# Optimization experiments

Hardware: AMD Instinct MI355X
Metric: run time of the kernel (lower is better)

The kernel has to match this reference:

```python
import jax, jax.numpy as jnp
import numpy as np

N_QUBITS = 4
N_LAYERS = 2
DIM = 2 ** N_QUBITS  # 16
B = 65536


def _apply_1q(state, U, wire):
    # state: (B,) + (2,)*N_QUBITS complex64; U: (2,2) complex. Wire 0 = most significant (PennyLane order).
    s = jnp.moveaxis(state, wire + 1, -1)
    s = jnp.einsum('...j,ij->...i', s, U)
    return jnp.moveaxis(s, -1, wire + 1)


def _apply_cnot(state, control, target):
    s = jnp.moveaxis(state, (control + 1, target + 1), (-2, -1))
    s = jnp.concatenate([s[..., 0:1, :], s[..., 1:2, ::-1]], axis=-2)
    return jnp.moveaxis(s, (-2, -1), (control + 1, target + 1))


def _rot_matrix(phi, th, om):
    # qml.Rot(phi, theta, omega) = RZ(om) RY(th) RZ(phi)
    c = jnp.cos(th / 2)
    sn = jnp.sin(th / 2)
    ep = jnp.exp(-0.5j * (phi + om).astype(jnp.complex64))
    em = jnp.exp(0.5j * (phi - om).astype(jnp.complex64))
    row0 = jnp.stack([ep * c, -em * sn])
    row1 = jnp.stack([jnp.conj(em) * sn, jnp.conj(ep) * c])
    return jnp.stack([row0, row1])


def _strongly_entangling(state, theta):
    # PennyLane StronglyEntanglingLayers, default ranges r_l = (l % (n-1)) + 1, CNOT imprimitive ring
    for l in range(N_LAYERS):
        for w in range(N_QUBITS):
            U = _rot_matrix(theta[l, w, 0], theta[l, w, 1], theta[l, w, 2])
            state = _apply_1q(state, U, w)
        r = (l % (N_QUBITS - 1)) + 1
        for w in range(N_QUBITS):
            state = _apply_cnot(state, w, (w + r) % N_QUBITS)
    return state


def _encode(x, W1, b1, W2, b2):
    v = x.reshape(x.shape[0], -1) @ W1 + b1
    v = jax.nn.relu(v)
    v = v @ W2 + b2
    v = jnp.nan_to_num(v, nan=0.0, posinf=1.0, neginf=-1.0)
    v = jnp.tanh(v)
    nrm = jnp.linalg.norm(v, axis=-1, keepdims=True)
    return v / jnp.maximum(nrm, 1e-8)  # F.normalize(p=2, eps=1e-8)


def _prepare_state(v, theta):
    # AmplitudeEmbedding(normalize=True): renormalize, embed as amplitudes
    v = v / jnp.linalg.norm(v, axis=-1, keepdims=True)
    state = v.astype(jnp.complex64).reshape((v.shape[0],) + (2,) * N_QUBITS)
    return _strongly_entangling(state, theta)


def setup_inputs() -> dict:
    key = jax.random.key(0)
    k = jax.random.split(key, 7)
    return {
        'img_a': jax.random.normal(k[0], (B, 1, 28, 28), dtype=jnp.float32),
        'img_b': jax.random.normal(k[1], (B, 1, 28, 28), dtype=jnp.float32),
        'W1': 0.05 * jax.random.normal(k[2], (784, 64), dtype=jnp.float32),
        'b1': 0.05 * jax.random.normal(k[3], (64,), dtype=jnp.float32),
        'W2': 0.05 * jax.random.normal(k[4], (64, 16), dtype=jnp.float32),
        'b2': 0.05 * jax.random.normal(k[5], (16,), dtype=jnp.float32),
        'theta': 0.05 * jax.random.normal(k[6], (N_LAYERS, N_QUBITS, 3), dtype=jnp.float32),
    }


def reference(img_a, img_b, W1, b1, W2, b2, theta):
    theta_safe = jnp.nan_to_num(theta, nan=0.0, posinf=1.0, neginf=-1.0)
    va = _encode(img_a, W1, b1, W2, b2)
    vb = _encode(img_b, W1, b1, W2, b2)
    sa = _prepare_state(va, theta_safe).reshape(-1, DIM)
    sb = _prepare_state(vb, theta_safe).reshape(-1, DIM)
    # SWAP test: p0 = (1 + |<a|b>|^2)/2  =>  clamp(2*p0 - 1, 0, 1) = clip(|<a|b>|^2, 0, 1)
    ov = jnp.einsum('bd,bd->b', jnp.conj(sa), sb)
    fid = jnp.clip(jnp.abs(ov) ** 2, 0.0, 1.0)
    return fid.astype(jnp.float32)
```

## Files before the change

### kernel.cpp

```cpp
#include <hip/hip_runtime.h>


#define KDIM   784
#define HDIM   64
#define KSTEPS 25
#define W1S_ELEMS (KSTEPS * 4 * 64 * 8)
#define W1S_BYTES (W1S_ELEMS * 2)

typedef float  f32x4  __attribute__((ext_vector_type(4)));
typedef short  bf16x8 __attribute__((ext_vector_type(8)));

__device__ __forceinline__ unsigned short f2bf(float f) {
  unsigned u = __float_as_uint(f);
  u += 0x7fffu + ((u >> 16) & 1u);
  return (unsigned short)(u >> 16);
}

__device__ __forceinline__ float bf2f(unsigned short h) {
  return __uint_as_float(((unsigned)h) << 16);
}

__device__ __forceinline__ bf16x8 cvt8(f32x4 lo, f32x4 hi) {
  bf16x8 r;
  r[0] = (short)f2bf(lo[0]); r[1] = (short)f2bf(lo[1]);
  r[2] = (short)f2bf(lo[2]); r[3] = (short)f2bf(lo[3]);
  r[4] = (short)f2bf(hi[0]); r[5] = (short)f2bf(hi[1]);
  r[6] = (short)f2bf(hi[2]); r[7] = (short)f2bf(hi[3]);
  return r;
}

__device__ __forceinline__ float tanh_fast(float x) {
  float e = __expf(2.0f * x);
  return 1.0f - 2.0f / (e + 1.0f);
}

__global__ __launch_bounds__(256)
void prep_kernel(const float* __restrict__ W1, const float* __restrict__ W2,
                 unsigned short* __restrict__ w1s, float* __restrict__ w2t) {
  int tid = blockIdx.x * 256 + threadIdx.x;
  if (tid < W1S_ELEMS) {
    int j  = tid & 7;
    int l  = (tid >> 3) & 63;
    int st = tid >> 9;
    int s  = st >> 2;
    int t  = st & 3;
    int k  = s * 32 + (l >> 4) * 8 + j;
    int n  = t * 16 + (l & 15);
    float v = (k < KDIM) ? W1[k * HDIM + n] : 0.0f;
    w1s[tid] = f2bf(v);
  }
  if (tid < HDIM * 16) {
    int c = tid >> 6;
    int k = tid & 63;
    w2t[c * HDIM + k] = W2[k * 16 + c];
  }
}

__global__ __launch_bounds__(256, 4)
void qcm_kernel(const float* __restrict__ img_a, const float* __restrict__ img_b,
                const float* __restrict__ b1,    const float* __restrict__ b2,
                const unsigned short* __restrict__ w1s,
                const float* __restrict__ w2t,
                float* __restrict__ out) {
  __shared__ __attribute__((aligned(16))) unsigned short lds_h[128][72];

  const int tid  = threadIdx.x;
  const int wave = tid >> 6;
  const int lane = tid & 63;
  const int m    = lane & 15;
  const int quad = lane >> 4;
  const int p0   = blockIdx.x * 64 + wave * 16;

  const float* rowA = img_a + (size_t)(p0 + m) * KDIM;
  const float* rowB = img_b + (size_t)(p0 + m) * KDIM;
  const int koff = quad * 8;

  f32x4 accA[4], accB[4];
  #pragma unroll
  for (int t = 0; t < 4; ++t) {
    accA[t][0] = accA[t][1] = accA[t][2] = accA[t][3] = 0.0f;
    accB[t][0] = accB[t][1] = accB[t][2] = accB[t][3] = 0.0f;
  }

  const int4* bwl = (const int4*)w1s + lane;
  f32x4 z4; z4[0] = z4[1] = z4[2] = z4[3] = 0.0f;

  f32x4 c0 = *(const f32x4*)(rowA + koff);
  f32x4 c1 = *(const f32x4*)(rowA + koff + 4);
  f32x4 c2 = *(const f32x4*)(rowB + koff);
  f32x4 c3 = *(const f32x4*)(rowB + koff + 4);

  for (int s = 0; s < KSTEPS; ++s) {
    int4 w0 = bwl[s * 256];
    int4 w1 = bwl[s * 256 + 64];
    int4 w2 = bwl[s * 256 + 128];
    int4 w3 = bwl[s * 256 + 192];

    f32x4 n0 = z4, n1 = z4, n2 = z4, n3 = z4;
    if (s < 23) {
      const int kb = (s + 1) * 32 + koff;
      n0 = *(const f32x4*)(rowA + kb);
      n1 = *(const f32x4*)(rowA + kb + 4);
      n2 = *(const f32x4*)(rowB + kb);
      n3 = *(const f32x4*)(rowB + kb + 4);
    } else if (s == 23) {
      if (quad < 2) {
        const int kb = 768 + koff;
        n0 = *(const f32x4*)(rowA + kb);
        n1 = *(const f32x4*)(rowA + kb + 4);
        n2 = *(const f32x4*)(rowB + kb);
        n3 = *(const f32x4*)(rowB + kb + 4);
      }
    }

    bf16x8 fa = cvt8(c0, c1);
    bf16x8 fb = cvt8(c2, c3);

    bf16x8 wf0 = __builtin_bit_cast(bf16x8, w0);
    bf16x8 wf1 = __builtin_bit_cast(bf16x8, w1);
    bf16x8 wf2 = __builtin_bit_cast(bf16x8, w2);
    bf16x8 wf3 = __builtin_bit_cast(bf16x8, w3);
    accA[0] = __builtin_amdgcn_mfma_f32_16x16x32_bf16(fa, wf0, accA[0], 0, 0, 0);
    accB[0] = __builtin_amdgcn_mfma_f32_16x16x32_bf16(fb, wf0, accB[0], 0, 0, 0);
    accA[1] = __builtin_amdgcn_mfma_f32_16x16x32_bf16(fa, wf1, accA[1], 0, 0, 0);
    accB[1] = __builtin_amdgcn_mfma_f32_16x16x32_bf16(fb, wf1, accB[1], 0, 0, 0);
    accA[2] = __builtin_amdgcn_mfma_f32_16x16x32_bf16(fa, wf2, accA[2], 0, 0, 0);
    accB[2] = __builtin_amdgcn_mfma_f32_16x16x32_bf16(fb, wf2, accB[2], 0, 0, 0);
    accA[3] = __builtin_amdgcn_mfma_f32_16x16x32_bf16(fa, wf3, accA[3], 0, 0, 0);
    accB[3] = __builtin_amdgcn_mfma_f32_16x16x32_bf16(fb, wf3, accB[3], 0, 0, 0);

    c0 = n0; c1 = n1; c2 = n2; c3 = n3;
  }

  #pragma unroll
  for (int t = 0; t < 4; ++t) {
    float bias = b1[t * 16 + m];
    const int ra = wave * 32;
    #pragma unroll
    for (int j = 0; j < 4; ++j) {
      float ha = fmaxf(accA[t][j] + bias, 0.0f);
      float hb = fmaxf(accB[t][j] + bias, 0.0f);
      lds_h[ra +      quad * 4 + j][t * 16 + m] = f2bf(ha);
      lds_h[ra + 16 + quad * 4 + j][t * 16 + m] = f2bf(hb);
    }
  }
  __syncthreads();

  const int p = tid >> 2;
  const int q = tid & 3;
  const int wsrc = p >> 4;
  const int r = p & 15;
  const unsigned short* ha_row = &lds_h[wsrc * 32 + r][0];
  const unsigned short* hb_row = &lds_h[wsrc * 32 + 16 + r][0];

  float za[4], zb[4];
  #pragma unroll
  for (int i = 0; i < 4; ++i) { za[i] = b2[q * 4 + i]; zb[i] = za[i]; }

  for (int k = 0; k < HDIM; k += 4) {
    uint2 ua = *(const uint2*)(ha_row + k);
    uint2 ub = *(const uint2*)(hb_row + k);
    float a0 = bf2f((unsigned short)(ua.x & 0xffff));
    float a1 = bf2f((unsigned short)(ua.x >> 16));
    float a2 = bf2f((unsigned short)(ua.y & 0xffff));
    float a3 = bf2f((unsigned short)(ua.y >> 16));
    float b0v = bf2f((unsigned short)(ub.x & 0xffff));
    float b1v = bf2f((unsigned short)(ub.x >> 16));
    float b2v = bf2f((unsigned short)(ub.y & 0xffff));
    float b3v = bf2f((unsigned short)(ub.y >> 16));
    #pragma unroll
    for (int i = 0; i < 4; ++i) {
      f32x4 wv = *(const f32x4*)(w2t + (q * 4 + i) * HDIM + k);
      za[i] += a0 * wv[0] + a1 * wv[1] + a2 * wv[2] + a3 * wv[3];
      zb[i] += b0v * wv[0] + b1v * wv[1] + b2v * wv[2] + b3v * wv[3];
    }
  }

  float d = 0.0f, na2 = 0.0f, nb2 = 0.0f;
  #pragma unroll
  for (int i = 0; i < 4; ++i) {
    float ua = tanh_fast(za[i]);
    float ub = tanh_fast(zb[i]);
    d   += ua * ub;
    na2 += ua * ua;
    nb2 += ub * ub;
  }
  d   += __shfl_xor(d, 1);   d   += __shfl_xor(d, 2);
  na2 += __shfl_xor(na2, 1); na2 += __shfl_xor(na2, 2);
  nb2 += __shfl_xor(nb2, 1); nb2 += __shfl_xor(nb2, 2);

  if (q == 0) {
    float den = fmaxf(sqrtf(na2), 1e-8f) * fmaxf(sqrtf(nb2), 1e-8f);
    float ov  = d / den;
    float fid = ov * ov;
    out[blockIdx.x * 64 + p] = fminf(fid, 1.0f);
  }
}

extern "C" void kernel_launch(void* const* d_in, const int* in_sizes, int n_in,
                              void* d_out, int out_size, void* d_ws, size_t ws_size,
                              hipStream_t stream) {
  const float* img_a = (const float*)d_in[0];
  const float* img_b = (const float*)d_in[1];
  const float* W1    = (const float*)d_in[2];
  const float* b1    = (const float*)d_in[3];
  const float* W2    = (const float*)d_in[4];
  const float* b2    = (const float*)d_in[5];

  unsigned short* w1s = (unsigned short*)d_ws;
  float* w2t = (float*)((char*)d_ws + W1S_BYTES);

  prep_kernel<<<(W1S_ELEMS + 255) / 256, 256, 0, stream>>>(W1, W2, w1s, w2t);

  const int n_pairs = out_size;
  qcm_kernel<<<n_pairs / 64, 256, 0, stream>>>(img_a, img_b, b1, b2, w1s, w2t,
                                               (float*)d_out);
}
```

Measured before the change: 116.9 us.

## Pack A and B rows into one MFMA tile to halve per-wave work

Each wave now handles 8 pairs, putting the img_a rows in MFMA rows 0-7 and the img_b rows in rows 8-15. That halves the accumulators and in-flight loads per thread, and launch bounds are raised to 8 blocks per CU with twice as many blocks. The aim is more occupancy and memory parallelism for this bandwidth-bound stream of images. The trade-off is twice the W1 fragment loads from cache per pair, and the second-layer stage is re-split over 8 threads per pair.

```diff
diff --git a/kernel.cpp b/kernel.cpp
--- a/kernel.cpp
+++ b/kernel.cpp
@@ -56,39 +56,36 @@
   }
 }
 
-__global__ __launch_bounds__(256, 4)
+__global__ __launch_bounds__(256, 8)
 void qcm_kernel(const float* __restrict__ img_a, const float* __restrict__ img_b,
                 const float* __restrict__ b1,    const float* __restrict__ b2,
                 const unsigned short* __restrict__ w1s,
                 const float* __restrict__ w2t,
                 float* __restrict__ out) {
-  __shared__ __attribute__((aligned(16))) unsigned short lds_h[128][72];
+  __shared__ __attribute__((aligned(16))) unsigned short lds_h[64][72];
 
   const int tid  = threadIdx.x;
   const int wave = tid >> 6;
   const int lane = tid & 63;
   const int m    = lane & 15;
   const int quad = lane >> 4;
-  const int p0   = blockIdx.x * 64 + wave * 16;
-
-  const float* rowA = img_a + (size_t)(p0 + m) * KDIM;
-  const float* rowB = img_b + (size_t)(p0 + m) * KDIM;
+  const int p0   = blockIdx.x * 32 + wave * 8;
+
+  const float* row = (m < 8)
+      ? (img_a + (size_t)(p0 + m)     * KDIM)
+      : (img_b + (size_t)(p0 + m - 8) * KDIM);
   const int koff = quad * 8;
 
-  f32x4 accA[4], accB[4];
+  f32x4 acc[4];
   #pragma unroll
-  for (int t = 0; t < 4; ++t) {
-    accA[t][0] = accA[t][1] = accA[t][2] = accA[t][3] = 0.0f;
-    accB[t][0] = accB[t][1] = accB[t][2] = accB[t][3] = 0.0f;
-  }
+  for (int t = 0; t < 4; ++t)
+    acc[t][0] = acc[t][1] = acc[t][2] = acc[t][3] = 0.0f;
 
   const int4* bwl = (const int4*)w1s + lane;
   f32x4 z4; z4[0] = z4[1] = z4[2] = z4[3] = 0.0f;
 
-  f32x4 c0 = *(const f32x4*)(rowA + koff);
-  f32x4 c1 = *(const f32x4*)(rowA + koff + 4);
-  f32x4 c2 = *(const f32x4*)(rowB + koff);
-  f32x4 c3 = *(const f32x4*)(rowB + koff + 4);
+  f32x4 c0 = *(const f32x4*)(row + koff);
+  f32x4 c1 = *(const f32x4*)(row + koff + 4);
 
   for (int s = 0; s < KSTEPS; ++s) {
     int4 w0 = bwl[s * 256];
@@ -96,66 +93,53 @@
     int4 w2 = bwl[s * 256 + 128];
     int4 w3 = bwl[s * 256 + 192];
 
-    f32x4 n0 = z4, n1 = z4, n2 = z4, n3 = z4;
+    f32x4 n0 = z4, n1 = z4;
     if (s < 23) {
       const int kb = (s + 1) * 32 + koff;
-      n0 = *(const f32x4*)(rowA + kb);
-      n1 = *(const f32x4*)(rowA + kb + 4);
-      n2 = *(const f32x4*)(rowB + kb);
-      n3 = *(const f32x4*)(rowB + kb + 4);
+      n0 = *(const f32x4*)(row + kb);
+      n1 = *(const f32x4*)(row + kb + 4);
     } else if (s == 23) {
       if (quad < 2) {
-        const int kb = 768 + koff;
-        n0 = *(const f32x4*)(rowA + kb);
-        n1 = *(const f32x4*)(rowA + kb + 4);
-        n2 = *(const f32x4*)(rowB + kb);
-        n3 = *(const f32x4*)(rowB + kb + 4);
+        n0 = *(const f32x4*)(row + 768 + koff);
+        n1 = *(const f32x4*)(row + 768 + koff + 4);
       }
     }
 
     bf16x8 fa = cvt8(c0, c1);
-    bf16x8 fb = cvt8(c2, c3);
-
-    bf16x8 wf0 = __builtin_bit_cast(bf16x8, w0);
-    bf16x8 wf1 = __builtin_bit_cast(bf16x8, w1);
-    bf16x8 wf2 = __builtin_bit_cast(bf16x8, w2);
-    bf16x8 wf3 = __builtin_bit_cast(bf16x8, w3);
-    accA[0] = __builtin_amdgcn_mfma_f32_16x16x32_bf16(fa, wf0, accA[0], 0, 0, 0);
-    accB[0] = __builtin_amdgcn_mfma_f32_16x16x32_bf16(fb, wf0, accB[0], 0, 0, 0);
-    accA[1] = __builtin_amdgcn_mfma_f32_16x16x32_bf16(fa, wf1, accA[1], 0, 0, 0);
-    accB[1] = __builtin_amdgcn_mfma_f32_16x16x32_bf16(fb, wf1, accB[1], 0, 0, 0);
-    accA[2] = __builtin_amdgcn_mfma_f32_16x16x32_bf16(fa, wf2, accA[2], 0, 0, 0);
-    accB[2] = __builtin_amdgcn_mfma_f32_16x16x32_bf16(fb, wf2, accB[2], 0, 0, 0);
-    accA[3] = __builtin_amdgcn_mfma_f32_16x16x32_bf16(fa, wf3, accA[3], 0, 0, 0);
-    accB[3] = __builtin_amdgcn_mfma_f32_16x16x32_bf16(fb, wf3, accB[3], 0, 0, 0);
-
-    c0 = n0; c1 = n1; c2 = n2; c3 = n3;
+
+    acc[0] = __builtin_amdgcn_mfma_f32_16x16x32_bf16(
+        fa, __builtin_bit_cast(bf16x8, w0), acc[0], 0, 0, 0);
+    acc[1] = __builtin_amdgcn_mfma_f32_16x16x32_bf16(
+        fa, __builtin_bit_cast(bf16x8, w1), acc[1], 0, 0, 0);
+    acc[2] = __builtin_amdgcn_mfma_f32_16x16x32_bf16(
+        fa, __builtin_bit_cast(bf16x8, w2), acc[2], 0, 0, 0);
+    acc[3] = __builtin_amdgcn_mfma_f32_16x16x32_bf16(
+        fa, __builtin_bit_cast(bf16x8, w3), acc[3], 0, 0, 0);
+
+    c0 = n0; c1 = n1;
   }
 
   #pragma unroll
   for (int t = 0; t < 4; ++t) {
     float bias = b1[t * 16 + m];
-    const int ra = wave * 32;
     #pragma unroll
     for (int j = 0; j < 4; ++j) {
-      float ha = fmaxf(accA[t][j] + bias, 0.0f);
-      float hb = fmaxf(accB[t][j] + bias, 0.0f);
-      lds_h[ra +      quad * 4 + j][t * 16 + m] = f2bf(ha);
-      lds_h[ra + 16 + quad * 4 + j][t * 16 + m] = f2bf(hb);
+      float h = fmaxf(acc[t][j] + bias, 0.0f);
+      lds_h[wave * 16 + quad * 4 + j][t * 16 + m] = f2bf(h);
     }
   }
   __syncthreads();
 
-  const int p = tid >> 2;
-  const int q = tid & 3;
-  const int wsrc = p >> 4;
-  const int r = p & 15;
-  const unsigned short* ha_row = &lds_h[wsrc * 32 + r][0];
-  const unsigned short* hb_row = &lds_h[wsrc * 32 + 16 + r][0];
-
-  float za[4], zb[4];
-  #pragma unroll
-  for (int i = 0; i < 4; ++i) { za[i] = b2[q * 4 + i]; zb[i] = za[i]; }
+  const int p = tid >> 3;
+  const int q = tid & 7;
+  const int wsrc = p >> 3;
+  const int r = p & 7;
+  const unsigned short* ha_row = &lds_h[wsrc * 16 + r][0];
+  const unsigned short* hb_row = &lds_h[wsrc * 16 + 8 + r][0];
+
+  float za[2], zb[2];
+  za[0] = b2[q * 2];     zb[0] = za[0];
+  za[1] = b2[q * 2 + 1]; zb[1] = za[1];
 
   for (int k = 0; k < HDIM; k += 4) {
     uint2 ua = *(const uint2*)(ha_row + k);
@@ -169,8 +153,8 @@
     float b2v = bf2f((unsigned short)(ub.y & 0xffff));
     float b3v = bf2f((unsigned short)(ub.y >> 16));
     #pragma unroll
-    for (int i = 0; i < 4; ++i) {
-      f32x4 wv = *(const f32x4*)(w2t + (q * 4 + i) * HDIM + k);
+    for (int i = 0; i < 2; ++i) {
+      f32x4 wv = *(const f32x4*)(w2t + (q * 2 + i) * HDIM + k);
       za[i] += a0 * wv[0] + a1 * wv[1] + a2 * wv[2] + a3 * wv[3];
       zb[i] += b0v * wv[0] + b1v * wv[1] + b2v * wv[2] + b3v * wv[3];
     }
@@ -178,22 +162,22 @@
 
   float d = 0.0f, na2 = 0.0f, nb2 = 0.0f;
   #pragma unroll
-  for (int i = 0; i < 4; ++i) {
+  for (int i = 0; i < 2; ++i) {
     float ua = tanh_fast(za[i]);
     float ub = tanh_fast(zb[i]);
     d   += ua * ub;
     na2 += ua * ua;
     nb2 += ub * ub;
   }
-  d   += __shfl_xor(d, 1);   d   += __shfl_xor(d, 2);
-  na2 += __shfl_xor(na2, 1); na2 += __shfl_xor(na2, 2);
-  nb2 += __shfl_xor(nb2, 1); nb2 += __shfl_xor(nb2, 2);
+  d   += __shfl_xor(d, 1);   d   += __shfl_xor(d, 2);   d   += __shfl_xor(d, 4);
+  na2 += __shfl_xor(na2, 1); na2 += __shfl_xor(na2, 2); na2 += __shfl_xor(na2, 4);
+  nb2 += __shfl_xor(nb2, 1); nb2 += __shfl_xor(nb2, 2); nb2 += __shfl_xor(nb2, 4);
 
   if (q == 0) {
     float den = fmaxf(sqrtf(na2), 1e-8f) * fmaxf(sqrtf(nb2), 1e-8f);
     float ov  = d / den;
     float fid = ov * ov;
-    out[blockIdx.x * 64 + p] = fminf(fid, 1.0f);
+    out[blockIdx.x * 32 + p] = fminf(fid, 1.0f);
   }
 }
 
@@ -213,6 +197,6 @@
   prep_kernel<<<(W1S_ELEMS + 255) / 256, 256, 0, stream>>>(W1, W2, w1s, w2t);
 
   const int n_pairs = out_size;
-  qcm_kernel<<<n_pairs / 64, 256, 0, stream>>>(img_a, img_b, b1, b2, w1s, w2t,
+  qcm_kernel<<<n_pairs / 32, 256, 0, stream>>>(img_a, img_b, b1, b2, w1s, w2t,
                                                (float*)d_out);
 }
```

New measurement: 134.7 us. 15.3% more time.

## Stage bf16 W1 tiles in LDS per 1024-thread block and deepen input prefetch

Applied to the files above, without the earlier changes.

Blocks grow from 256 to 1024 threads. Each block first copies the whole pre-swizzled bf16 W1 (about 100KB) into shared memory, and the MFMA loop reads weight fragments from LDS instead of global or L2 memory. The image-row loads are now prefetched two k-steps ahead. The goal is to cut repeated global weight traffic and hide input load latency in a memory-bound GEMV-like pass. In exchange, the large LDS footprint limits each CU to one block, and every block pays a prologue copy plus a barrier before streaming begins.

```diff
diff --git a/kernel.cpp b/kernel.cpp
--- a/kernel.cpp
+++ b/kernel.cpp
@@ -6,6 +6,7 @@
 #define KSTEPS 25
 #define W1S_ELEMS (KSTEPS * 4 * 64 * 8)
 #define W1S_BYTES (W1S_ELEMS * 2)
+#define W1S_INT4  (W1S_BYTES / 16)
 
 typedef float  f32x4  __attribute__((ext_vector_type(4)));
 typedef short  bf16x8 __attribute__((ext_vector_type(8)));
@@ -32,6 +33,30 @@
 __device__ __forceinline__ float tanh_fast(float x) {
   float e = __expf(2.0f * x);
   return 1.0f - 2.0f / (e + 1.0f);
+}
+
+__device__ __forceinline__ void load_a(const float* __restrict__ rowA,
+                                       const float* __restrict__ rowB,
+                                       int st, int koff, int quad,
+                                       f32x4& r0, f32x4& r1,
+                                       f32x4& r2, f32x4& r3) {
+  f32x4 z; z[0] = z[1] = z[2] = z[3] = 0.0f;
+  r0 = r1 = r2 = r3 = z;
+  if (st < 24) {
+    const int kb = st * 32 + koff;
+    r0 = *(const f32x4*)(rowA + kb);
+    r1 = *(const f32x4*)(rowA + kb + 4);
+    r2 = *(const f32x4*)(rowB + kb);
+    r3 = *(const f32x4*)(rowB + kb + 4);
+  } else if (st == 24) {
+    if (quad < 2) {
+      const int kb = 768 + koff;
+      r0 = *(const f32x4*)(rowA + kb);
+      r1 = *(const f32x4*)(rowA + kb + 4);
+      r2 = *(const f32x4*)(rowB + kb);
+      r3 = *(const f32x4*)(rowB + kb + 4);
+    }
+  }
 }
 
 __global__ __launch_bounds__(256)
@@ -56,20 +81,32 @@
   }
 }
 
-__global__ __launch_bounds__(256, 4)
+__global__ __launch_bounds__(1024, 4)
 void qcm_kernel(const float* __restrict__ img_a, const float* __restrict__ img_b,
                 const float* __restrict__ b1,    const float* __restrict__ b2,
                 const unsigned short* __restrict__ w1s,
                 const float* __restrict__ w2t,
                 float* __restrict__ out) {
-  __shared__ __attribute__((aligned(16))) unsigned short lds_h[128][72];
-
-  const int tid  = threadIdx.x;
+  __shared__ __attribute__((aligned(16))) char smem[W1S_BYTES];
+
+  const int tid = threadIdx.x;
+
+  {
+    const int4* src = (const int4*)w1s;
+    int4* dst = (int4*)smem;
+    #pragma unroll
+    for (int i = 0; i < 7; ++i) {
+      int idx = tid + i * 1024;
+      if (idx < W1S_INT4) dst[idx] = src[idx];
+    }
+  }
+  __syncthreads();
+
   const int wave = tid >> 6;
   const int lane = tid & 63;
   const int m    = lane & 15;
   const int quad = lane >> 4;
-  const int p0   = blockIdx.x * 64 + wave * 16;
+  const int p0   = blockIdx.x * 256 + wave * 16;
 
   const float* rowA = img_a + (size_t)(p0 + m) * KDIM;
   const float* rowB = img_b + (size_t)(p0 + m) * KDIM;
@@ -82,55 +119,49 @@
     accB[t][0] = accB[t][1] = accB[t][2] = accB[t][3] = 0.0f;
   }
 
-  const int4* bwl = (const int4*)w1s + lane;
-  f32x4 z4; z4[0] = z4[1] = z4[2] = z4[3] = 0.0f;
-
-  f32x4 c0 = *(const f32x4*)(rowA + koff);
-  f32x4 c1 = *(const f32x4*)(rowA + koff + 4);
-  f32x4 c2 = *(const f32x4*)(rowB + koff);
-  f32x4 c3 = *(const f32x4*)(rowB + koff + 4);
+  const int4* wl = (const int4*)smem;
+
+  f32x4 t0, t1, t2, t3;
+  load_a(rowA, rowB, 0, koff, quad, t0, t1, t2, t3);
+  f32x4 pa0, pa1, pb0, pb1;
+  load_a(rowA, rowB, 1, koff, quad, pa0, pa1, pb0, pb1);
+  bf16x8 curA = cvt8(t0, t1);
+  bf16x8 curB = cvt8(t2, t3);
 
   for (int s = 0; s < KSTEPS; ++s) {
-    int4 w0 = bwl[s * 256];
-    int4 w1 = bwl[s * 256 + 64];
-    int4 w2 = bwl[s * 256 + 128];
-    int4 w3 = bwl[s * 256 + 192];
-
-    f32x4 n0 = z4, n1 = z4, n2 = z4, n3 = z4;
-    if (s < 23) {
-      const int kb = (s + 1) * 32 + koff;
-      n0 = *(const f32x4*)(rowA + kb);
-      n1 = *(const f32x4*)(rowA + kb + 4);
-      n2 = *(const f32x4*)(rowB + kb);
-      n3 = *(const f32x4*)(rowB + kb + 4);
-    } else if (s == 23) {
-      if (quad < 2) {
-        const int kb = 768 + koff;
-        n0 = *(const f32x4*)(rowA + kb);
-        n1 = *(const f32x4*)(rowA + kb + 4);
-        n2 = *(const f32x4*)(rowB + kb);
-        n3 = *(const f32x4*)(rowB + kb + 4);
-      }
-    }
-
-    bf16x8 fa = cvt8(c0, c1);
-    bf16x8 fb = cvt8(c2, c3);
-
-    bf16x8 wf0 = __builtin_bit_cast(bf16x8, w0);
-    bf16x8 wf1 = __builtin_bit_cast(bf16x8, w1);
-    bf16x8 wf2 = __builtin_bit_cast(bf16x8, w2);
-    bf16x8 wf3 = __builtin_bit_cast(bf16x8, w3);
-    accA[0] = __builtin_amdgcn_mfma_f32_16x16x32_bf16(fa, wf0, accA[0], 0, 0, 0);
-    accB[0] = __builtin_amdgcn_mfma_f32_16x16x32_bf16(fb, wf0, accB[0], 0, 0, 0);
-    accA[1] = __builtin_amdgcn_mfma_f32_16x16x32_bf16(fa, wf1, accA[1], 0, 0, 0);
-    accB[1] = __builtin_amdgcn_mfma_f32_16x16x32_bf16(fb, wf1, accB[1], 0, 0, 0);
-    accA[2] = __builtin_amdgcn_mfma_f32_16x16x32_bf16(fa, wf2, accA[2], 0, 0, 0);
-    accB[2] = __builtin_amdgcn_mfma_f32_16x16x32_bf16(fb, wf2, accB[2], 0, 0, 0);
-    accA[3] = __builtin_amdgcn_mfma_f32_16x16x32_bf16(fa, wf3, accA[3], 0, 0, 0);
-    accB[3] = __builtin_amdgcn_mfma_f32_16x16x32_bf16(fb, wf3, accB[3], 0, 0, 0);
-
-    c0 = n0; c1 = n1; c2 = n2; c3 = n3;
-  }
+    f32x4 f0, f1, f2, f3;
+    load_a(rowA, rowB, s + 2, koff, quad, f0, f1, f2, f3);
+
+    const int base = s * 256 + lane;
+    int4 w0 = wl[base];
+    int4 w1 = wl[base + 64];
+    int4 w2 = wl[base + 128];
+    int4 w3 = wl[base + 192];
+
+    accA[0] = __builtin_amdgcn_mfma_f32_16x16x32_bf16(
+        curA, __builtin_bit_cast(bf16x8, w0), accA[0], 0, 0, 0);
+    accB[0] = __builtin_amdgcn_mfma_f32_16x16x32_bf16(
+        curB, __builtin_bit_cast(bf16x8, w0), accB[0], 0, 0, 0);
+    accA[1] = __builtin_amdgcn_mfma_f32_16x16x32_bf16(
+        curA, __builtin_bit_cast(bf16x8, w1), accA[1], 0, 0, 0);
+    accB[1] = __builtin_amdgcn_mfma_f32_16x16x32_bf16(
+        curB, __builtin_bit_cast(bf16x8, w1), accB[1], 0, 0, 0);
+    accA[2] = __builtin_amdgcn_mfma_f32_16x16x32_bf16(
+        curA, __builtin_bit_cast(bf16x8, w2), accA[2], 0, 0, 0);
+    accB[2] = __builtin_amdgcn_mfma_f32_16x16x32_bf16(
+        curB, __builtin_bit_cast(bf16x8, w2), accB[2], 0, 0, 0);
+    accA[3] = __builtin_amdgcn_mfma_f32_16x16x32_bf16(
+        curA, __builtin_bit_cast(bf16x8, w3), accA[3], 0, 0, 0);
+    accB[3] = __builtin_amdgcn_mfma_f32_16x16x32_bf16(
+        curB, __builtin_bit_cast(bf16x8, w3), accB[3], 0, 0, 0);
+
+    curA = cvt8(pa0, pa1);
+    curB = cvt8(pb0, pb1);
+    pa0 = f0; pa1 = f1; pb0 = f2; pb1 = f3;
+  }
+
+  __syncthreads();
+  unsigned short (*lds_h)[72] = (unsigned short(*)[72])smem;
 
   #pragma unroll
   for (int t = 0; t < 4; ++t) {
@@ -193,7 +224,7 @@
     float den = fmaxf(sqrtf(na2), 1e-8f) * fmaxf(sqrtf(nb2), 1e-8f);
     float ov  = d / den;
     float fid = ov * ov;
-    out[blockIdx.x * 64 + p] = fminf(fid, 1.0f);
+    out[blockIdx.x * 256 + p] = fminf(fid, 1.0f);
   }
 }
 
@@ -213,6 +244,6 @@
   prep_kernel<<<(W1S_ELEMS + 255) / 256, 256, 0, stream>>>(W1, W2, w1s, w2t);
 
   const int n_pairs = out_size;
-  qcm_kernel<<<n_pairs / 64, 256, 0, stream>>>(img_a, img_b, b1, b2, w1s, w2t,
-                                               (float*)d_out);
-}
+  qcm_kernel<<<n_pairs / 256, 1024, 0, stream>>>(img_a, img_b, b1, b2, w1s, w2t,
+                                                 (float*)d_out);
+}
```

After: 117.9 us. No clear change (+0.9%).

## Deepen GEMM load pipeline to two stages ahead with register ring buffer

Applied to the files above, without the earlier changes.

The K-loop now prefetches both image rows and W1 fragments two steps ahead into a three-slot register ring, instead of only the image rows one step ahead. The loop is fully unrolled and fenced with sched_barriers so the loads are issued early. The aim is to keep more global loads in flight and hide memory latency in this bandwidth-bound encoder. The extra registers are accepted by lowering the launch-bounds occupancy hint from 4 to 3, so fewer waves may be resident to hide latency.

```diff
diff --git a/kernel.cpp b/kernel.cpp
--- a/kernel.cpp
+++ b/kernel.cpp
@@ -56,7 +56,7 @@
   }
 }
 
-__global__ __launch_bounds__(256, 4)
+__global__ __launch_bounds__(256, 3)
 void qcm_kernel(const float* __restrict__ img_a, const float* __restrict__ img_b,
                 const float* __restrict__ b1,    const float* __restrict__ b2,
                 const unsigned short* __restrict__ w1s,
@@ -83,43 +83,48 @@
   }
 
   const int4* bwl = (const int4*)w1s + lane;
-  f32x4 z4; z4[0] = z4[1] = z4[2] = z4[3] = 0.0f;
-
-  f32x4 c0 = *(const f32x4*)(rowA + koff);
-  f32x4 c1 = *(const f32x4*)(rowA + koff + 4);
-  f32x4 c2 = *(const f32x4*)(rowB + koff);
-  f32x4 c3 = *(const f32x4*)(rowB + koff + 4);
-
+
+  f32x4 A0[3], A1[3], B0[3], B1[3];
+  int4  W0[3], W1r[3], W2r[3], W3r[3];
+
+  auto issue = [&](int st, int sl) __attribute__((always_inline)) {
+    if (st > 24) return;
+    const float *pa, *pb;
+    if (st < 24) {
+      pa = rowA + st * 32 + koff;
+      pb = rowB + st * 32 + koff;
+    } else {
+      const int off = (quad < 2) ? (768 + koff) : 0;
+      pa = rowA + off;
+      pb = rowB + off;
+    }
+    A0[sl] = *(const f32x4*)pa;
+    A1[sl] = *(const f32x4*)(pa + 4);
+    B0[sl] = *(const f32x4*)pb;
+    B1[sl] = *(const f32x4*)(pb + 4);
+    W0[sl]  = bwl[st * 256];
+    W1r[sl] = bwl[st * 256 + 64];
+    W2r[sl] = bwl[st * 256 + 128];
+    W3r[sl] = bwl[st * 256 + 192];
+  };
+
+  issue(0, 0);
+  issue(1, 1);
+  __builtin_amdgcn_sched_barrier(0);
+
+  #pragma unroll
   for (int s = 0; s < KSTEPS; ++s) {
-    int4 w0 = bwl[s * 256];
-    int4 w1 = bwl[s * 256 + 64];
-    int4 w2 = bwl[s * 256 + 128];
-    int4 w3 = bwl[s * 256 + 192];
-
-    f32x4 n0 = z4, n1 = z4, n2 = z4, n3 = z4;
-    if (s < 23) {
-      const int kb = (s + 1) * 32 + koff;
-      n0 = *(const f32x4*)(rowA + kb);
-      n1 = *(const f32x4*)(rowA + kb + 4);
-      n2 = *(const f32x4*)(rowB + kb);
-      n3 = *(const f32x4*)(rowB + kb + 4);
-    } else if (s == 23) {
-      if (quad < 2) {
-        const int kb = 768 + koff;
-        n0 = *(const f32x4*)(rowA + kb);
-        n1 = *(const f32x4*)(rowA + kb + 4);
-        n2 = *(const f32x4*)(rowB + kb);
-        n3 = *(const f32x4*)(rowB + kb + 4);
-      }
-    }
-
-    bf16x8 fa = cvt8(c0, c1);
-    bf16x8 fb = cvt8(c2, c3);
-
-    bf16x8 wf0 = __builtin_bit_cast(bf16x8, w0);
-    bf16x8 wf1 = __builtin_bit_cast(bf16x8, w1);
-    bf16x8 wf2 = __builtin_bit_cast(bf16x8, w2);
-    bf16x8 wf3 = __builtin_bit_cast(bf16x8, w3);
+    issue(s + 2, (s + 2) % 3);
+    __builtin_amdgcn_sched_barrier(0);
+
+    const int sc = s % 3;
+    bf16x8 fa = cvt8(A0[sc], A1[sc]);
+    bf16x8 fb = cvt8(B0[sc], B1[sc]);
+
+    bf16x8 wf0 = __builtin_bit_cast(bf16x8, W0[sc]);
+    bf16x8 wf1 = __builtin_bit_cast(bf16x8, W1r[sc]);
+    bf16x8 wf2 = __builtin_bit_cast(bf16x8, W2r[sc]);
+    bf16x8 wf3 = __builtin_bit_cast(bf16x8, W3r[sc]);
     accA[0] = __builtin_amdgcn_mfma_f32_16x16x32_bf16(fa, wf0, accA[0], 0, 0, 0);
     accB[0] = __builtin_amdgcn_mfma_f32_16x16x32_bf16(fb, wf0, accB[0], 0, 0, 0);
     accA[1] = __builtin_amdgcn_mfma_f32_16x16x32_bf16(fa, wf1, accA[1], 0, 0, 0);
@@ -128,8 +133,6 @@
     accB[2] = __builtin_amdgcn_mfma_f32_16x16x32_bf16(fb, wf2, accB[2], 0, 0, 0);
     accA[3] = __builtin_amdgcn_mfma_f32_16x16x32_bf16(fa, wf3, accA[3], 0, 0, 0);
     accB[3] = __builtin_amdgcn_mfma_f32_16x16x32_bf16(fb, wf3, accB[3], 0, 0, 0);
-
-    c0 = n0; c1 = n1; c2 = n2; c3 = n3;
   }
 
   #pragma unroll
```

New measurement: 112.6 us. 3.6% less time.
